# Kernel tuning notes

Measured on AMD Instinct MI355X. Metric: run time of the kernel, lower is better.

The kernel has to match this reference:

```python
import jax, jax.numpy as jnp
import numpy as np

# ---- static config (mirrors CE defaults) ----
PS = 7        # patch size
WS = 27       # search window (per side)
S0 = 4        # query stride (stride0)
KS = 100      # k_s: top-k kept by search
KA = 100      # k_a: top-k used for aggregation
SCALE = 10.0  # softmax_scale
CI = 16       # inter_channels


def conv2d(x, w, b, pad):
    y = jax.lax.conv_general_dilated(
        x, w, (1, 1), [(pad, pad), (pad, pad)],
        dimension_numbers=("NCHW", "OIHW", "NCHW"))
    return y + b[None, :, None, None]


def all_patches(v):
    """[T,C,H,W] -> [T, H*W, C*PS*PS]; top-left anchored PSxPS patches,
    edge-clamped at the border (dnls-style bounded patch extraction)."""
    t, c, h, w = v.shape
    ii = jnp.clip(jnp.arange(h)[:, None] + jnp.arange(PS)[None, :], 0, h - 1)
    jj = jnp.clip(jnp.arange(w)[:, None] + jnp.arange(PS)[None, :], 0, w - 1)
    p = v[:, :, ii][:, :, :, :, jj]          # [T,C,H,PS,W,PS]
    p = p.transpose(0, 2, 4, 1, 3, 5)        # [T,H,W,C,PS,PS]
    return p.reshape(t, h * w, c * PS * PS)


def setup_inputs():
    key = jax.random.key(0)
    ks = jax.random.split(key, 4)
    vid = jax.random.normal(ks[0], (4, 64, 128, 128), jnp.float32)
    g_w = jax.random.normal(ks[1], (CI, 64, 3, 3), jnp.float32) * 0.05
    g_b = jnp.zeros((CI,), jnp.float32)
    theta_w = jax.random.normal(ks[2], (CI, 64, 1, 1), jnp.float32) * 0.1
    theta_b = jnp.zeros((CI,), jnp.float32)
    return {"vid": vid, "g_w": g_w, "g_b": g_b,
            "theta_w": theta_w, "theta_b": theta_b}


def reference(vid, g_w, g_b, theta_w, theta_b):
    t, c, h, w = vid.shape
    nH, nW = h // S0, w // S0
    Q, N = nH * nW, h * w

    # feature extraction (g -> search features, theta -> aggregation values)
    v1 = conv2d(vid, g_w, g_b, 1)          # [T,CI,H,W]
    v2 = conv2d(vid, theta_w, theta_b, 0)  # [T,CI,H,W]

    # windowed k-NN patch search: query grid (stride0) vs all keys (stride1=1)
    P1 = all_patches(v1)                                    # [T,N,D]
    qis = jnp.arange(nH) * S0
    qjs = jnp.arange(nW) * S0
    qflat = (qis[:, None] * w + qjs[None, :]).reshape(-1)   # [Q]
    Pq = P1[:, qflat]                                       # [T,Q,D]
    scores = jnp.einsum("tqd,tnd->tqn", Pq, P1)             # [T,Q,N]

    off = jnp.arange(WS) - WS // 2
    ci = jnp.clip(qis[:, None] + off, 0, h - 1)             # [nH,WS]
    cj = jnp.clip(qjs[:, None] + off, 0, w - 1)             # [nW,WS]
    cand = (ci[:, None, :, None] * w + cj[None, :, None, :]).reshape(Q, WS * WS)
    dists = jnp.take_along_axis(scores, cand[None], axis=2)  # [T,Q,WS*WS]

    d_k, widx = jax.lax.top_k(dists, KS)                    # [T,Q,KS]
    inds = jnp.take_along_axis(jnp.broadcast_to(cand[None], dists.shape),
                               widx, axis=2)                # flat key positions

    # top-k softmax aggregation weights
    wgt = jax.nn.softmax(d_k[..., :KA] * SCALE, axis=-1)    # [T,Q,KA]
    inds_a = inds[..., :KA]

    # wpsum: weighted sum of value patches gathered at neighbor indices,
    # expressed as sparse-scatter matrix @ dense patch matrix
    A = jnp.zeros((t, Q, N), scores.dtype).at[
        jnp.arange(t)[:, None, None],
        jnp.arange(Q)[None, :, None],
        inds_a].add(wgt)                                    # [T,Q,N]
    P2 = all_patches(v2)                                    # [T,N,D]
    z = jnp.einsum("tqn,tnd->tqd", A, P2)                   # [T,Q,CI*PS*PS]

    # ifold: scatter-add overlapping patches + count normalization
    z = z.reshape(t, Q, CI, PS, PS).transpose(0, 2, 1, 3, 4)
    z = z.reshape(t, CI, Q * PS * PS)
    ri = jnp.clip(qis[:, None] + jnp.arange(PS), 0, h - 1)  # [nH,PS]
    rj = jnp.clip(qjs[:, None] + jnp.arange(PS), 0, w - 1)  # [nW,PS]
    pix = (ri[:, None, :, None] * w + rj[None, :, None, :]).reshape(-1)
    Y = jnp.zeros((t, CI, N), z.dtype).at[:, :, pix].add(z)
    Zc = jnp.zeros((N,), z.dtype).at[pix].add(1.0)
    y = (Y / Zc).reshape(t, CI, h, w)
    return y
```

## Files before the change

### kernel.cpp

```cpp
#include <hip/hip_runtime.h>
#include <hip/hip_bf16.h>

#define T_ 4
#define C_ 64
#define H_ 128
#define W_ 128
#define CI_ 16
#define PS_ 7
#define NC_ 729
#define NCP_ 732
#define S0_ 4
#define KS_ 100
#define NQ_ 1024
#define SCALE_ 10.0f
#define HW_ (H_*W_)
#define RW_ 45
#define LCAP_ 768
#define CB_ 8

typedef float v2f __attribute__((ext_vector_type(2)));
#if __has_builtin(__builtin_elementwise_fma)
#define VFMA(a, b, c) __builtin_elementwise_fma((a), (b), (c))
#else
#define VFMA(a, b, c) ((a) * (b) + (c))
#endif

__device__ __forceinline__ float4 colfix(float4 r, bool loB, bool hiB) {
  float4 o;
  o.x = loB ? 0.f : (hiB ? r.y : r.x);
  o.y = loB ? r.x : (hiB ? r.z : r.y);
  o.z = loB ? r.y : (hiB ? r.w : r.z);
  o.w = loB ? r.z : (hiB ? 0.f : r.w);
  return o;
}

__global__ __launch_bounds__(128, 1) void conv_fused_kernel(
    const float* __restrict__ vid, const float* __restrict__ gw,
    const float* __restrict__ gb, const float* __restrict__ tw,
    const float* __restrict__ tb, float4* __restrict__ v1cs,
    float4* __restrict__ v2cs) {
  __shared__ float wls[C_ * 9 * 4];
  __shared__ float tls[C_ * 4];
  const int tid = threadIdx.x;
  const int g = blockIdx.y, t = blockIdx.z;
  for (int m = tid; m < C_ * 9 * 4; m += 128) {
    int co = m & 3, ck = m >> 2;
    wls[m] = gw[((size_t)(g * 4 + co) * C_) * 9 + ck];
  }
  for (int m = tid; m < C_ * 4; m += 128) {
    int o = m & 3, c = m >> 2;
    tls[m] = tw[(g * 4 + o) * C_ + c];
  }
  __syncthreads();
  const int ti0 = (blockIdx.x >> 3) * 16, tj0 = (blockIdx.x & 7) * 16;
  const int u = tid >> 3, v = tid & 7;
  const int i = ti0 + u, j0 = tj0 + 2 * v;
  const int c0 = j0 - 1;
  const int c0c = min(max(c0, 0), W_ - 4);
  const bool loB = (c0 < 0), hiB = (c0 > W_ - 4);
  const int rm1 = max(i - 1, 0), rp1 = min(i + 1, H_ - 1);
  const float mk0 = (i > 0) ? 1.f : 0.f;
  const float mk2 = (i < H_ - 1) ? 1.f : 0.f;
  const int o0 = rm1 * W_ + c0c, o1 = i * W_ + c0c, o2 = rp1 * W_ + c0c;

  float accA[4], accB[4], acc1A[4], acc1B[4];
#pragma unroll
  for (int co = 0; co < 4; ++co) {
    accA[co] = gb[g * 4 + co]; accB[co] = gb[g * 4 + co];
    acc1A[co] = tb[g * 4 + co]; acc1B[co] = tb[g * 4 + co];
  }

  const float* vb = vid + ((size_t)t * C_) * HW_;
#pragma unroll 1
  for (int cb = 0; cb < C_; cb += CB_) {
    float4 r[CB_][3];
#pragma unroll
    for (int c = 0; c < CB_; ++c) {
      const float* p = vb + (size_t)(cb + c) * HW_;
      r[c][0] = *(const float4*)(p + o0);
      r[c][1] = *(const float4*)(p + o1);
      r[c][2] = *(const float4*)(p + o2);
    }
#pragma unroll
    for (int c = 0; c < CB_; ++c) {
      float4 f0 = colfix(r[c][0], loB, hiB);
      float4 f1 = colfix(r[c][1], loB, hiB);
      float4 f2 = colfix(r[c][2], loB, hiB);
      f0.x *= mk0; f0.y *= mk0; f0.z *= mk0; f0.w *= mk0;
      f2.x *= mk2; f2.y *= mk2; f2.z *= mk2; f2.w *= mk2;
      const float* wc = &wls[(cb + c) * 36];
      const float* tc = &tls[(cb + c) * 4];
      float e0[4] = {f0.x, f0.y, f0.z, f0.w};
      float e1[4] = {f1.x, f1.y, f1.z, f1.w};
      float e2[4] = {f2.x, f2.y, f2.z, f2.w};
#pragma unroll
      for (int co = 0; co < 4; ++co) {
        acc1A[co] = fmaf(tc[co], e1[1], acc1A[co]);
        acc1B[co] = fmaf(tc[co], e1[2], acc1B[co]);
      }
#pragma unroll
      for (int kj = 0; kj < 3; ++kj) {
#pragma unroll
        for (int co = 0; co < 4; ++co) {
          accA[co] = fmaf(wc[(0 * 3 + kj) * 4 + co], e0[kj],     accA[co]);
          accB[co] = fmaf(wc[(0 * 3 + kj) * 4 + co], e0[kj + 1], accB[co]);
          accA[co] = fmaf(wc[(1 * 3 + kj) * 4 + co], e1[kj],     accA[co]);
          accB[co] = fmaf(wc[(1 * 3 + kj) * 4 + co], e1[kj + 1], accB[co]);
          accA[co] = fmaf(wc[(2 * 3 + kj) * 4 + co], e2[kj],     accA[co]);
          accB[co] = fmaf(wc[(2 * 3 + kj) * 4 + co], e2[kj + 1], accB[co]);
        }
      }
    }
  }
  const size_t o = ((size_t)g * T_ + t) * HW_ + i * W_ + j0;
  v1cs[o]     = make_float4(accA[0], accA[1], accA[2], accA[3]);
  v1cs[o + 1] = make_float4(accB[0], accB[1], accB[2], accB[3]);
  v2cs[o]     = make_float4(acc1A[0], acc1A[1], acc1A[2], acc1A[3]);
  v2cs[o + 1] = make_float4(acc1B[0], acc1B[1], acc1B[2], acc1B[3]);
}

__global__ __launch_bounds__(512, 2) void dist_kernel(
    const float4* __restrict__ v1cs, float* __restrict__ out,
    int cbase, int nch) {
  __shared__ float4 Rs[2][2048];
  const int tid = threadIdx.x;
  const int t = blockIdx.y;
  const int qi0 = (blockIdx.x >> 3) * 16, qj0 = (blockIdx.x & 7) * 16;
  const int w = tid >> 6, lane = tid & 63;
  const int pr = w >> 2, dj = (w & 3) * 4;
  const int rbase = 8 * pr;
  const int qi_p = qi0 + rbase;
  const int qj = qj0 + dj;
  const int la = lane >> 1, bg = lane & 1;
  const int b_lo = max(13 - qj, 0);
  const int bs = bg ? 13 : b_lo;
  const int a_lo0 = max(13 - qi_p, 0);
  const int a_lo1 = max(9 - qi_p, 0);
  const bool compute_ok = (la < 31);

  int soff[4];
#pragma unroll
  for (int k = 0; k < 4; ++k) {
    int p = min(tid + 512 * k, RW_ * RW_ - 1);
    int uu = p / RW_, vv = p - uu * RW_;
    int row = min(max(qi0 - 13 + uu, 0), H_ - 1);
    int col = min(max(qj0 - 13 + vv, 0), W_ - 1);
    soff[k] = row * W_ + col;
  }

  v2f acc0[14], acc1[14];
#pragma unroll
  for (int j = 0; j < 14; ++j) { acc0[j] = (v2f){0.f, 0.f}; acc1[j] = (v2f){0.f, 0.f}; }

  float4 st[4];
  {
    const float4* src = v1cs + ((size_t)cbase * T_ + t) * HW_;
#pragma unroll
    for (int k = 0; k < 4; ++k) st[k] = src[soff[k]];
  }
  int cur = 0;
#pragma unroll 1
  for (int ci = 0; ci < nch; ++ci) {
    float4* buf = &Rs[cur][0];
#pragma unroll
    for (int k = 0; k < 4; ++k) buf[tid + 512 * k] = st[k];
    if (ci + 1 < nch) {
      const float4* src = v1cs + ((size_t)(cbase + ci + 1) * T_ + t) * HW_;
#pragma unroll
      for (int k = 0; k < 4; ++k) st[k] = src[soff[k]];
    }
    __syncthreads();
    if (compute_ok) {
#pragma unroll 1
      for (int r = 0; r < 7; ++r) {
        v2f q0lo[7], q0hi[7], q1lo[7], q1hi[7];
        const float4* q0row = &buf[(rbase + 13 + r) * RW_ + dj + 13];
#pragma unroll
        for (int s = 0; s < 7; ++s) {
          float4 qq = q0row[s];
          q0lo[s] = (v2f){qq.x, qq.y};
          q0hi[s] = (v2f){qq.z, qq.w};
          float4 q2 = q0row[4 * RW_ + s];
          q1lo[s] = (v2f){q2.x, q2.y};
          q1hi[s] = (v2f){q2.z, q2.w};
        }
        const float4* crow = &buf[(rbase + la + r) * RW_ + dj + bs];
#pragma unroll
        for (int y = 0; y < 20; ++y) {
          float4 vv4 = crow[y];
          v2f vlo = (v2f){vv4.x, vv4.y}, vhi = (v2f){vv4.z, vv4.w};
          const int s_lo = (y > 13) ? (y - 13) : 0;
          const int s_hi = (y < 6) ? y : 6;
#pragma unroll
          for (int s = s_lo; s <= s_hi; ++s) {
            int j = y - s;
            acc0[j] = VFMA(q0lo[s], vlo, acc0[j]);
            acc0[j] = VFMA(q0hi[s], vhi, acc0[j]);
            acc1[j] = VFMA(q1lo[s], vlo, acc1[j]);
            acc1[j] = VFMA(q1hi[s], vhi, acc1[j]);
          }
        }
      }
    }
    cur ^= 1;
  }
  if (compute_ok) {
    const int q0q = ((qi_p >> 2) << 5) + (qj >> 2);
    if (la >= a_lo0 && la <= 26) {
      float* o = out + ((size_t)t * NQ_ + q0q) * NCP_ + la * 27 + bs;
#pragma unroll
      for (int j = 0; j < 14; ++j) o[j] = acc0[j].x + acc0[j].y;
    }
    const int a1 = la - 4;
    if (a1 >= a_lo1 && a1 <= 26) {
      float* o = out + ((size_t)t * NQ_ + (q0q + 32)) * NCP_ + a1 * 27 + bs;
#pragma unroll
      for (int j = 0; j < 14; ++j) o[j] = acc1[j].x + acc1[j].y;
    }
  }
}

__global__ __launch_bounds__(256) void select_kernel(
    const float* __restrict__ distA, const float* __restrict__ distB, int dual,
    int* __restrict__ sel_n, float* __restrict__ sel_w,
    float* __restrict__ wsum_out) {
  __shared__ float dist[NC_];
  __shared__ unsigned int ukey[NC_];
  __shared__ float redf[4];
  __shared__ unsigned int hist[256];
  __shared__ int lk[LCAP_];
  __shared__ unsigned int lkey[LCAP_];
  __shared__ unsigned int scal[6];

  const int tid = threadIdx.x;
  const int lane = tid & 63, wid = tid >> 6;
  const int q = blockIdx.x, t = blockIdx.y;
  const int qi = (q >> 5) * S0_, qj = (q & 31) * S0_;
  const int a_lo = max(13 - qi, 0), b_lo = max(13 - qj, 0);
  const size_t base = ((size_t)t * NQ_ + q) * NCP_;

  for (int h = tid; h < 256; h += 256) hist[h] = 0;
  if (tid == 0) { scal[2] = 0; scal[3] = 0; }
  float lmax = -INFINITY;
  if (a_lo == 0 && b_lo == 0) {
    if (tid < 182) {
      float4 d4 = *(const float4*)(distA + base + 4 * tid);
      if (dual) {
        float4 b4 = *(const float4*)(distB + base + 4 * tid);
        d4.x += b4.x; d4.y += b4.y; d4.z += b4.z; d4.w += b4.w;
      }
      float dv[4] = {d4.x, d4.y, d4.z, d4.w};
#pragma unroll
      for (int e = 0; e < 4; ++e) {
        int k = 4 * tid + e;
        float d = dv[e];
        dist[k] = d;
        unsigned int u = __float_as_uint(d);
        ukey[k] = u ^ (((unsigned int)((int)u >> 31)) | 0x80000000u);
        lmax = fmaxf(lmax, d);
      }
    } else if (tid == 182) {
      float d = distA[base + 728];
      if (dual) d += distB[base + 728];
      dist[728] = d;
      unsigned int u = __float_as_uint(d);
      ukey[728] = u ^ (((unsigned int)((int)u >> 31)) | 0x80000000u);
      lmax = d;
    }
  } else {
    for (int k = tid; k < NC_; k += 256) {
      int aa = k / 27, bb = k - aa * 27;
      int kk = max(aa, a_lo) * 27 + max(bb, b_lo);
      float d = distA[base + kk];
      if (dual) d += distB[base + kk];
      dist[k] = d;
      unsigned int u = __float_as_uint(d);
      ukey[k] = u ^ (((unsigned int)((int)u >> 31)) | 0x80000000u);
      lmax = fmaxf(lmax, d);
    }
  }
#pragma unroll
  for (int off = 32; off > 0; off >>= 1)
    lmax = fmaxf(lmax, __shfl_down(lmax, off, 64));
  if (lane == 0) redf[wid] = lmax;
  __syncthreads();
  const float dmax = fmaxf(fmaxf(redf[0], redf[1]), fmaxf(redf[2], redf[3]));
  for (int k = tid; k < NC_; k += 256) atomicAdd(&hist[ukey[k] >> 24], 1u);
  __syncthreads();
  if (wid == 0) {
    int s4 = (int)(hist[lane * 4] + hist[lane * 4 + 1] + hist[lane * 4 + 2] + hist[lane * 4 + 3]);
    int s = s4;
#pragma unroll
    for (int off = 1; off < 64; off <<= 1) {
      int o = __shfl_down(s, off, 64);
      if (lane + off < 64) s += o;
    }
    int above = s - s4;
    if (above < KS_ && s >= KS_) {
      int run = above;
#pragma unroll
      for (int bb = 3; bb >= 0; --bb) {
        int h = (int)hist[lane * 4 + bb];
        if (run + h >= KS_) { scal[0] = (unsigned int)(lane * 4 + bb); scal[1] = (unsigned int)run; break; }
        run += h;
      }
    }
  }
  __syncthreads();
  const unsigned int beta = scal[0];
  const int run = (int)scal[1];
  for (int h = tid; h < 256; h += 256) hist[h] = 0;
  __syncthreads();
  for (int k = tid; k < NC_; k += 256)
    if ((ukey[k] >> 24) == beta) atomicAdd(&hist[(ukey[k] >> 16) & 0xFFu], 1u);
  __syncthreads();
  if (wid == 0) {
    int s4 = (int)(hist[lane * 4] + hist[lane * 4 + 1] + hist[lane * 4 + 2] + hist[lane * 4 + 3]);
    int s = s4;
#pragma unroll
    for (int off = 1; off < 64; off <<= 1) {
      int o = __shfl_down(s, off, 64);
      if (lane + off < 64) s += o;
    }
    int above = run + s - s4;
    if (above < KS_ && run + s >= KS_) {
      int r2 = above;
#pragma unroll
      for (int bb = 3; bb >= 0; --bb) {
        int h = (int)hist[lane * 4 + bb];
        if (r2 + h >= KS_) { scal[4] = (unsigned int)(lane * 4 + bb); scal[5] = (unsigned int)r2; break; }
        r2 += h;
      }
    }
  }
  __syncthreads();
  const unsigned int beta2 = scal[4];
  const int run2 = (int)scal[5];
  const size_t outb = ((size_t)t * NQ_ + q) * KS_;
  float lsum = 0.f;
  for (int k = tid; k < NC_; k += 256) {
    unsigned int key = ukey[k];
    unsigned int bin = key >> 24;
    bool sel = false, bdry = false;
    if (bin > beta) sel = true;
    else if (bin == beta) {
      unsigned int b2 = (key >> 16) & 0xFFu;
      if (b2 > beta2) sel = true;
      else if (b2 == beta2) bdry = true;
    }
    if (sel) {
      unsigned int slot = atomicAdd(&scal[2], 1u);
      int aa = k / 27, bb = k - aa * 27;
      int ni = min(max(qi + aa - 13, 0), H_ - 1);
      int nj = min(max(qj + bb - 13, 0), W_ - 1);
      float wv = __expf(SCALE_ * (dist[k] - dmax));
      sel_n[outb + slot] = (ni << 7) | nj;
      sel_w[outb + slot] = wv;
      lsum += wv;
    } else if (bdry) {
      unsigned int pos = atomicAdd(&scal[3], 1u);
      if (pos < LCAP_) { lk[pos] = k; lkey[pos] = key; }
    }
  }
  __syncthreads();
  const int L = min((int)scal[3], LCAP_);
  for (int i = tid; i < L; i += 256) {
    unsigned int key = lkey[i];
    int k = lk[i];
    int cnt = run2;
    for (int m = 0; m < L; ++m)
      cnt += (int)((lkey[m] > key) || (lkey[m] == key && lk[m] < k));
    if (cnt < KS_) {
      unsigned int slot = atomicAdd(&scal[2], 1u);
      int aa = k / 27, bb = k - aa * 27;
      int ni = min(max(qi + aa - 13, 0), H_ - 1);
      int nj = min(max(qj + bb - 13, 0), W_ - 1);
      float wv = __expf(SCALE_ * (dist[k] - dmax));
      sel_n[outb + slot] = (ni << 7) | nj;
      sel_w[outb + slot] = wv;
      lsum += wv;
    }
  }
#pragma unroll
  for (int off = 32; off > 0; off >>= 1) lsum += __shfl_down(lsum, off, 64);
  __syncthreads();
  if (lane == 0) redf[wid] = lsum;
  __syncthreads();
  if (tid == 0) wsum_out[t * NQ_ + q] = (redf[0] + redf[1]) + (redf[2] + redf[3]);
}

__device__ __forceinline__ int cov_axis(int x) {
  int c = 0;
#pragma unroll
  for (int r = 0; r < 7; ++r) {
    if (x < H_ - 1) {
      int qb = x - r;
      c += (qb >= 0 && (qb & 3) == 0) ? 1 : 0;
    } else {
      c += (r >= 3) ? 1 : 0;
    }
  }
  return c;
}

__global__ __launch_bounds__(1024) void agg_kernel(
    const float4* __restrict__ v2cs, const int* __restrict__ sel_n,
    const float* __restrict__ sel_w, const float* __restrict__ wsum,
    float* __restrict__ Y) {
  __shared__ float4 Rs[RW_ * RW_];
  __shared__ int s_off[16][KS_];
  __shared__ float s_w[16][KS_];
  const int tid = threadIdx.x;
  const int t = blockIdx.y;
  const int qi0 = (blockIdx.x >> 3) * 16, qj0 = (blockIdx.x & 7) * 16;
  const int w = tid >> 6, lane = tid & 63;
  const int di = (w >> 2) * 4, dj = (w & 3) * 4;
  const int qi = qi0 + di, qj = qj0 + dj;
  const int q = ((qi >> 2) << 5) + (qj >> 2);
  const size_t base = ((size_t)t * NQ_ + q) * KS_;
  const float inv = 1.0f / wsum[t * NQ_ + q];
  for (int k = lane; k < KS_; k += 64) {
    int n = sel_n[base + k];
    int ni = n >> 7, nj = n & 127;
    s_off[w][k] = (ni - qi0 + 13) * RW_ + (nj - qj0 + 13);
    s_w[w][k] = sel_w[base + k] * inv;
  }
  const int r = lane / 7, s = lane - r * 7;
  const int myo = r * RW_ + s;
  const int oi = min(qi + r, H_ - 1), oj = min(qj + s, W_ - 1);
  const float invZ = 1.0f / (float)(cov_axis(oi) * cov_axis(oj));
#pragma unroll 1
  for (int cc = 0; cc < 4; ++cc) {
    __syncthreads();
    const float4* src = v2cs + ((size_t)cc * T_ + t) * HW_;
    for (int p = tid; p < RW_ * RW_; p += 1024) {
      int uu = p / RW_, vv = p - uu * RW_;
      int row = min(max(qi0 - 13 + uu, 0), H_ - 1);
      int col = min(max(qj0 - 13 + vv, 0), W_ - 1);
      Rs[p] = src[row * W_ + col];
    }
    __syncthreads();
    if (lane < 49) {
      float4 acc = make_float4(0.f, 0.f, 0.f, 0.f);
#pragma unroll 4
      for (int k = 0; k < KS_; ++k) {
        float wv = s_w[w][k];
        float4 v = Rs[s_off[w][k] + myo];
        acc.x = fmaf(wv, v.x, acc.x);
        acc.y = fmaf(wv, v.y, acc.y);
        acc.z = fmaf(wv, v.z, acc.z);
        acc.w = fmaf(wv, v.w, acc.w);
      }
      float* yb = Y + (((size_t)t * CI_ + cc * 4) * H_ + oi) * W_ + oj;
      atomicAdd(yb, acc.x * invZ);
      atomicAdd(yb + HW_, acc.y * invZ);
      atomicAdd(yb + 2 * HW_, acc.z * invZ);
      atomicAdd(yb + 3 * HW_, acc.w * invZ);
    }
  }
}

extern "C" void kernel_launch(void* const* d_in, const int* in_sizes, int n_in,
                              void* d_out, int out_size, void* d_ws, size_t ws_size,
                              hipStream_t stream) {
  const float* vid     = (const float*)d_in[0];
  const float* g_w     = (const float*)d_in[1];
  const float* g_b     = (const float*)d_in[2];
  const float* theta_w = (const float*)d_in[3];
  const float* theta_b = (const float*)d_in[4];
  float* Y = (float*)d_out;

  float* v1cs  = (float*)d_ws;
  float* v2cs  = v1cs + (size_t)4 * T_ * HW_ * 4;
  float* distG = v2cs + (size_t)4 * T_ * HW_ * 4;
  int*   sel_n = (int*)(distG + (size_t)T_ * NQ_ * NCP_);
  float* sel_w = (float*)(sel_n + (size_t)T_ * NQ_ * KS_);
  float* wsumv = sel_w + (size_t)T_ * NQ_ * KS_;
  float* distB = wsumv + (size_t)T_ * NQ_;

  const size_t need_dual =
      ((size_t)4 * T_ * HW_ * 4 * 2 + (size_t)T_ * NQ_ * NCP_ * 2 +
       (size_t)T_ * NQ_ * KS_ * 2 + (size_t)T_ * NQ_) * sizeof(float);
  const int dual = (ws_size >= need_dual) ? 1 : 0;

  hipMemsetAsync(Y, 0, (size_t)out_size * sizeof(float), stream);

  conv_fused_kernel<<<dim3(64, 4, T_), 128, 0, stream>>>(
      vid, g_w, g_b, theta_w, theta_b, (float4*)v1cs, (float4*)v2cs);
  if (dual) {
    dist_kernel<<<dim3(64, T_), 512, 0, stream>>>((const float4*)v1cs, distG, 0, 2);
    dist_kernel<<<dim3(64, T_), 512, 0, stream>>>((const float4*)v1cs, distB, 2, 2);
  } else {
    dist_kernel<<<dim3(64, T_), 512, 0, stream>>>((const float4*)v1cs, distG, 0, 4);
  }
  select_kernel<<<dim3(NQ_, T_), 256, 0, stream>>>(distG, distB, dual, sel_n, sel_w, wsumv);
  agg_kernel<<<dim3(64, T_), 1024, 0, stream>>>((const float4*)v2cs, sel_n, sel_w, wsumv, Y);
}
```

Before: 265.4 us.

## Split conv input channels across two block halves, summing partials downstream

The conv kernel now splits the 64 input channels into two halves. Each half runs in its own block and writes partial sums to separate buffers, which doubles the grid from 1024 to 2048 blocks. The dist and agg kernels add the two partial buffers as they load. This is meant to raise parallelism and occupancy in the conv stage, which previously launched only 1024 blocks of 128 threads. In exchange, the consumers read twice as much feature data and the workspace needed for the feature maps doubles, which can change whether the dual dist path is taken.

```diff
diff --git a/kernel.cpp b/kernel.cpp
--- a/kernel.cpp
+++ b/kernel.cpp
@@ -17,6 +17,7 @@
 #define RW_ 45
 #define LCAP_ 768
 #define CB_ 8
+#define CH_ 32
 
 typedef float v2f __attribute__((ext_vector_type(2)));
 #if __has_builtin(__builtin_elementwise_fma)
@@ -24,6 +25,10 @@
 #else
 #define VFMA(a, b, c) ((a) * (b) + (c))
 #endif
+
+__device__ __forceinline__ float4 f4add(float4 a, float4 b) {
+  return make_float4(a.x + b.x, a.y + b.y, a.z + b.z, a.w + b.w);
+}
 
 __device__ __forceinline__ float4 colfix(float4 r, bool loB, bool hiB) {
   float4 o;
@@ -37,19 +42,21 @@
 __global__ __launch_bounds__(128, 1) void conv_fused_kernel(
     const float* __restrict__ vid, const float* __restrict__ gw,
     const float* __restrict__ gb, const float* __restrict__ tw,
-    const float* __restrict__ tb, float4* __restrict__ v1cs,
-    float4* __restrict__ v2cs) {
-  __shared__ float wls[C_ * 9 * 4];
-  __shared__ float tls[C_ * 4];
+    const float* __restrict__ tb, float4* __restrict__ v1A,
+    float4* __restrict__ v1B, float4* __restrict__ v2A,
+    float4* __restrict__ v2B) {
+  __shared__ float wls[CH_ * 9 * 4];
+  __shared__ float tls[CH_ * 4];
   const int tid = threadIdx.x;
-  const int g = blockIdx.y, t = blockIdx.z;
-  for (int m = tid; m < C_ * 9 * 4; m += 128) {
+  const int g = blockIdx.y;
+  const int t = blockIdx.z & 3, half = blockIdx.z >> 2;
+  for (int m = tid; m < CH_ * 9 * 4; m += 128) {
     int co = m & 3, ck = m >> 2;
-    wls[m] = gw[((size_t)(g * 4 + co) * C_) * 9 + ck];
-  }
-  for (int m = tid; m < C_ * 4; m += 128) {
+    wls[m] = gw[((size_t)(g * 4 + co) * C_) * 9 + half * (CH_ * 9) + ck];
+  }
+  for (int m = tid; m < CH_ * 4; m += 128) {
     int o = m & 3, c = m >> 2;
-    tls[m] = tw[(g * 4 + o) * C_ + c];
+    tls[m] = tw[(g * 4 + o) * C_ + half * CH_ + c];
   }
   __syncthreads();
   const int ti0 = (blockIdx.x >> 3) * 16, tj0 = (blockIdx.x & 7) * 16;
@@ -66,13 +73,15 @@
   float accA[4], accB[4], acc1A[4], acc1B[4];
 #pragma unroll
   for (int co = 0; co < 4; ++co) {
-    accA[co] = gb[g * 4 + co]; accB[co] = gb[g * 4 + co];
-    acc1A[co] = tb[g * 4 + co]; acc1B[co] = tb[g * 4 + co];
-  }
-
-  const float* vb = vid + ((size_t)t * C_) * HW_;
+    float bg = half ? 0.f : gb[g * 4 + co];
+    float bt = half ? 0.f : tb[g * 4 + co];
+    accA[co] = bg; accB[co] = bg;
+    acc1A[co] = bt; acc1B[co] = bt;
+  }
+
+  const float* vb = vid + ((size_t)t * C_ + half * CH_) * HW_;
 #pragma unroll 1
-  for (int cb = 0; cb < C_; cb += CB_) {
+  for (int cb = 0; cb < CH_; cb += CB_) {
     float4 r[CB_][3];
 #pragma unroll
     for (int c = 0; c < CB_; ++c) {
@@ -112,16 +121,18 @@
       }
     }
   }
+  float4* v1o = half ? v1B : v1A;
+  float4* v2o = half ? v2B : v2A;
   const size_t o = ((size_t)g * T_ + t) * HW_ + i * W_ + j0;
-  v1cs[o]     = make_float4(accA[0], accA[1], accA[2], accA[3]);
-  v1cs[o + 1] = make_float4(accB[0], accB[1], accB[2], accB[3]);
-  v2cs[o]     = make_float4(acc1A[0], acc1A[1], acc1A[2], acc1A[3]);
-  v2cs[o + 1] = make_float4(acc1B[0], acc1B[1], acc1B[2], acc1B[3]);
+  v1o[o]     = make_float4(accA[0], accA[1], accA[2], accA[3]);
+  v1o[o + 1] = make_float4(accB[0], accB[1], accB[2], accB[3]);
+  v2o[o]     = make_float4(acc1A[0], acc1A[1], acc1A[2], acc1A[3]);
+  v2o[o + 1] = make_float4(acc1B[0], acc1B[1], acc1B[2], acc1B[3]);
 }
 
 __global__ __launch_bounds__(512, 2) void dist_kernel(
-    const float4* __restrict__ v1cs, float* __restrict__ out,
-    int cbase, int nch) {
+    const float4* __restrict__ v1A, const float4* __restrict__ v1B,
+    float* __restrict__ out, int cbase, int nch) {
   __shared__ float4 Rs[2][2048];
   const int tid = threadIdx.x;
   const int t = blockIdx.y;
@@ -154,9 +165,10 @@
 
   float4 st[4];
   {
-    const float4* src = v1cs + ((size_t)cbase * T_ + t) * HW_;
-#pragma unroll
-    for (int k = 0; k < 4; ++k) st[k] = src[soff[k]];
+    const float4* sA = v1A + ((size_t)cbase * T_ + t) * HW_;
+    const float4* sB = v1B + ((size_t)cbase * T_ + t) * HW_;
+#pragma unroll
+    for (int k = 0; k < 4; ++k) st[k] = f4add(sA[soff[k]], sB[soff[k]]);
   }
   int cur = 0;
 #pragma unroll 1
@@ -165,9 +177,10 @@
 #pragma unroll
     for (int k = 0; k < 4; ++k) buf[tid + 512 * k] = st[k];
     if (ci + 1 < nch) {
-      const float4* src = v1cs + ((size_t)(cbase + ci + 1) * T_ + t) * HW_;
-#pragma unroll
-      for (int k = 0; k < 4; ++k) st[k] = src[soff[k]];
+      const float4* sA = v1A + ((size_t)(cbase + ci + 1) * T_ + t) * HW_;
+      const float4* sB = v1B + ((size_t)(cbase + ci + 1) * T_ + t) * HW_;
+#pragma unroll
+      for (int k = 0; k < 4; ++k) st[k] = f4add(sA[soff[k]], sB[soff[k]]);
     }
     __syncthreads();
     if (compute_ok) {
@@ -404,9 +417,9 @@
 }
 
 __global__ __launch_bounds__(1024) void agg_kernel(
-    const float4* __restrict__ v2cs, const int* __restrict__ sel_n,
-    const float* __restrict__ sel_w, const float* __restrict__ wsum,
-    float* __restrict__ Y) {
+    const float4* __restrict__ v2A, const float4* __restrict__ v2B,
+    const int* __restrict__ sel_n, const float* __restrict__ sel_w,
+    const float* __restrict__ wsum, float* __restrict__ Y) {
   __shared__ float4 Rs[RW_ * RW_];
   __shared__ int s_off[16][KS_];
   __shared__ float s_w[16][KS_];
@@ -432,12 +445,14 @@
 #pragma unroll 1
   for (int cc = 0; cc < 4; ++cc) {
     __syncthreads();
-    const float4* src = v2cs + ((size_t)cc * T_ + t) * HW_;
+    const float4* sA = v2A + ((size_t)cc * T_ + t) * HW_;
+    const float4* sB = v2B + ((size_t)cc * T_ + t) * HW_;
     for (int p = tid; p < RW_ * RW_; p += 1024) {
       int uu = p / RW_, vv = p - uu * RW_;
       int row = min(max(qi0 - 13 + uu, 0), H_ - 1);
       int col = min(max(qj0 - 13 + vv, 0), W_ - 1);
-      Rs[p] = src[row * W_ + col];
+      const int so = row * W_ + col;
+      Rs[p] = f4add(sA[so], sB[so]);
     }
     __syncthreads();
     if (lane < 49) {
@@ -470,29 +485,37 @@
   const float* theta_b = (const float*)d_in[4];
   float* Y = (float*)d_out;
 
-  float* v1cs  = (float*)d_ws;
-  float* v2cs  = v1cs + (size_t)4 * T_ * HW_ * 4;
-  float* distG = v2cs + (size_t)4 * T_ * HW_ * 4;
+  const size_t VSZ = (size_t)4 * T_ * HW_ * 4;
+  float* v1A   = (float*)d_ws;
+  float* v1B   = v1A + VSZ;
+  float* v2A   = v1B + VSZ;
+  float* v2B   = v2A + VSZ;
+  float* distG = v2B + VSZ;
   int*   sel_n = (int*)(distG + (size_t)T_ * NQ_ * NCP_);
   float* sel_w = (float*)(sel_n + (size_t)T_ * NQ_ * KS_);
   float* wsumv = sel_w + (size_t)T_ * NQ_ * KS_;
   float* distB = wsumv + (size_t)T_ * NQ_;
 
   const size_t need_dual =
-      ((size_t)4 * T_ * HW_ * 4 * 2 + (size_t)T_ * NQ_ * NCP_ * 2 +
+      (VSZ * 4 + (size_t)T_ * NQ_ * NCP_ * 2 +
        (size_t)T_ * NQ_ * KS_ * 2 + (size_t)T_ * NQ_) * sizeof(float);
   const int dual = (ws_size >= need_dual) ? 1 : 0;
 
   hipMemsetAsync(Y, 0, (size_t)out_size * sizeof(float), stream);
 
-  conv_fused_kernel<<<dim3(64, 4, T_), 128, 0, stream>>>(
-      vid, g_w, g_b, theta_w, theta_b, (float4*)v1cs, (float4*)v2cs);
+  conv_fused_kernel<<<dim3(64, 4, 2 * T_), 128, 0, stream>>>(
+      vid, g_w, g_b, theta_w, theta_b,
+      (float4*)v1A, (float4*)v1B, (float4*)v2A, (float4*)v2B);
   if (dual) {
-    dist_kernel<<<dim3(64, T_), 512, 0, stream>>>((const float4*)v1cs, distG, 0, 2);
-    dist_kernel<<<dim3(64, T_), 512, 0, stream>>>((const float4*)v1cs, distB, 2, 2);
+    dist_kernel<<<dim3(64, T_), 512, 0, stream>>>(
+        (const float4*)v1A, (const float4*)v1B, distG, 0, 2);
+    dist_kernel<<<dim3(64, T_), 512, 0, stream>>>(
+        (const float4*)v1A, (const float4*)v1B, distB, 2, 2);
   } else {
-    dist_kernel<<<dim3(64, T_), 512, 0, stream>>>((const float4*)v1cs, distG, 0, 4);
+    dist_kernel<<<dim3(64, T_), 512, 0, stream>>>(
+        (const float4*)v1A, (const float4*)v1B, distG, 0, 4);
   }
   select_kernel<<<dim3(NQ_, T_), 256, 0, stream>>>(distG, distB, dual, sel_n, sel_w, wsumv);
-  agg_kernel<<<dim3(64, T_), 1024, 0, stream>>>((const float4*)v2cs, sel_n, sel_w, wsumv, Y);
-}
+  agg_kernel<<<dim3(64, T_), 1024, 0, stream>>>(
+      (const float4*)v2A, (const float4*)v2B, sel_n, sel_w, wsumv, Y);
+}
```

New measurement: 256.4 us. -3.4%, faster.
